# Kernel tuning notes

Measured on AMD Instinct MI355X. Metric: run time of the kernel, lower is better.

Reference implementation:

```python
import jax, jax.numpy as jnp
import numpy as np

MUL = 128          # multiplicity of 0e and 1o in left/output irreps
N_NODES = 131072   # graph nodes (batch dim)
INV_SQRT3 = 1.0 / np.sqrt(3.0)        # CG value for 0x1->1 and 1x1->0 (wigner 3j)
ALPHA = 1.0 / np.sqrt(2.0 * MUL)      # path_normalization='element': 2 paths of mul1*mul2=128 per output irrep
# effective per-instruction coefficients (CG * sqrt(2*l_out+1) component norm * ALPHA):
#   (0e,0e)->0e : 1 * 1 * ALPHA
#   (1o,1o)->0e : (1/sqrt(3)) * 1 * ALPHA
#   (0e,1o)->1o : (1/sqrt(3)) * sqrt(3) * ALPHA = ALPHA
#   (1o,0e)->1o : ALPHA


def setup_inputs() -> dict:
    key = jax.random.key(0)
    ks = jax.random.split(key, 7)
    x = jax.random.normal(ks[0], (N_NODES, 4 * MUL), jnp.float32)  # 128x0e + 128x1o -> dim 512
    y = jax.random.normal(ks[1], (N_NODES, 4), jnp.float32)        # 1x0e + 1x1o -> dim 4
    uni = lambda k: jax.random.uniform(k, (MUL, 1, MUL), jnp.float32, -1.0, 1.0)
    W1 = uni(ks[2])  # path (0e,0e)->0e
    W2 = uni(ks[3])  # path (0e,1o)->1o
    W3 = uni(ks[4])  # path (1o,0e)->1o
    W4 = uni(ks[5])  # path (1o,1o)->0e
    b = jax.random.uniform(ks[6], (MUL,), jnp.float32, -1.0, 1.0) / np.sqrt(MUL)
    return {"x": x, "y": y, "W1": W1, "W2": W2, "W3": W3, "W4": W4, "b": b}


def reference(x, y, W1, W2, W3, W4, b):
    n = x.shape[0]
    x0 = x[:, :MUL]                       # [N, 128]    scalars
    x1 = x[:, MUL:].reshape(n, MUL, 3)    # [N, 128, 3] vectors
    y0 = y[:, :1]                         # [N, 1]
    y1 = y[:, 1:].reshape(n, 1, 3)        # [N, 1, 3]
    # scalar output: (0e,0e)->0e and (1o,1o)->0e (inner product CG), plus bias
    out0 = ALPHA * (jnp.einsum('nu,nv,uvw->nw', x0, y0, W1)
                    + INV_SQRT3 * jnp.einsum('nui,nvi,uvw->nw', x1, y1, W4)) + b
    # vector output: (0e,1o)->1o and (1o,0e)->1o (identity CG)
    out1 = ALPHA * (jnp.einsum('nu,nvi,uvw->nwi', x0, y1, W2)
                    + jnp.einsum('nui,nv,uvw->nwi', x1, y0, W3))
    return jnp.concatenate([out0, out1.reshape(n, 3 * MUL)], axis=1)  # [N, 512]
```

## Files before the change

kernel.cpp:

```cpp
#include <hip/hip_runtime.h>

#define TILE_NODES 32
#define NBLOCKS 512

typedef __attribute__((ext_vector_type(4))) float f32x4;
typedef __attribute__((ext_vector_type(8))) __bf16 bf16x8;
typedef __attribute__((ext_vector_type(8))) unsigned short u16x8;

__device__ __forceinline__ unsigned short f2bf(float f) {
    unsigned u = __builtin_bit_cast(unsigned, f);
    u += 0x7fffu + ((u >> 16) & 1u);
    return (unsigned short)(u >> 16);
}

__global__ void build_bfrag_kernel(const float* __restrict__ W1,
                                   const float* __restrict__ W2,
                                   const float* __restrict__ W3,
                                   const float* __restrict__ W4,
                                   unsigned short* __restrict__ bfrag) {
    const float ALPHA = 0.0625f;
    const float A3    = 0.0625f * 0.57735026918962576f;
    int i = blockIdx.x * 256 + threadIdx.x;
    int j  = i & 7;
    int l  = (i >> 3) & 63;
    int ct = (i >> 9) & 7;
    int kt = (i >> 12) & 3;
    int T  = (i >> 14) & 3;
    int k   = kt * 32 + ((l >> 4) & 3) * 8 + j;
    int col = ct * 16 + (l & 15);
    const float* W = (T == 0) ? W1 : (T == 1) ? W2 : (T == 2) ? W3 : W4;
    float s = (T == 3) ? A3 : ALPHA;
    bfrag[i] = f2bf(s * W[k * 128 + col]);
}

__global__ __launch_bounds__(512, 2)
void o3tp_kernel(const float* __restrict__ x, const float* __restrict__ y,
                 const float* __restrict__ bias,
                 const unsigned short* __restrict__ bfrag,
                 float* __restrict__ out, int tiles_per_block) {
    __shared__ __align__(16) unsigned char smem[65536];
    const int tid = threadIdx.x;
    const int w   = tid >> 6;
    const int l   = tid & 63;
    const int lk  = l >> 4;
    const int lr  = l & 15;

    u16x8 bq[4][4];
    #pragma unroll
    for (int T = 0; T < 4; ++T)
        #pragma unroll
        for (int kt = 0; kt < 4; ++kt)
            bq[T][kt] = *(const u16x8*)(bfrag + (((T * 4 + kt) * 8 + w) << 9) + l * 8);
    const float bias_v = bias[w * 16 + lr];

    const int n_  = tid >> 4;
    const int G   = tid & 15;
    const int swz = (n_ & 7) << 4;

    const long tile0 = (long)blockIdx.x * tiles_per_block;

    f32x4 X0a, X0b, Ta, Tb, Tc, Td, Te, Tf;
    auto LOADS = [&](long tile) {
        const float* bp = x + (tile * TILE_NODES + n_) * 512;
        X0a = *(const f32x4*)(bp + 8 * G);
        X0b = *(const f32x4*)(bp + 8 * G + 4);
        const float* tp = bp + 128 + 24 * G;
        Ta = *(const f32x4*)(tp);      Tb = *(const f32x4*)(tp + 4);
        Tc = *(const f32x4*)(tp + 8);  Td = *(const f32x4*)(tp + 12);
        Te = *(const f32x4*)(tp + 16); Tf = *(const f32x4*)(tp + 20);
    };
    auto WRITE = [&](int buf) {
        unsigned char* base = smem + buf * 32768 + n_ * 256 + ((16 * G) ^ swz);
        u16x8 v;
        v[0] = f2bf(X0a[0]); v[1] = f2bf(X0a[1]); v[2] = f2bf(X0a[2]); v[3] = f2bf(X0a[3]);
        v[4] = f2bf(X0b[0]); v[5] = f2bf(X0b[1]); v[6] = f2bf(X0b[2]); v[7] = f2bf(X0b[3]);
        *(u16x8*)(base) = v;
        float t[24] = {Ta[0],Ta[1],Ta[2],Ta[3], Tb[0],Tb[1],Tb[2],Tb[3],
                       Tc[0],Tc[1],Tc[2],Tc[3], Td[0],Td[1],Td[2],Td[3],
                       Te[0],Te[1],Te[2],Te[3], Tf[0],Tf[1],Tf[2],Tf[3]};
        #pragma unroll
        for (int i3 = 0; i3 < 3; ++i3) {
            u16x8 u;
            #pragma unroll
            for (int up = 0; up < 8; ++up) u[up] = f2bf(t[3 * up + i3]);
            *(u16x8*)(base + (i3 + 1) * 8192) = u;
        }
    };

    LOADS(tile0);
    WRITE(0);

    for (int it = 0; it < tiles_per_block; ++it) {
        const long tile = tile0 + it;
        __syncthreads();
        if (it + 1 < tiles_per_block) LOADS(tile + 1);

        const unsigned char* ab = smem + (it & 1) * 32768;
        f32x4 M1[2] = {}, M2[2] = {}, M3[3][2] = {}, M4[3][2] = {};
        #pragma unroll
        for (int c = 0; c < 4; ++c) {
            u16x8 ar[2][4];
            #pragma unroll
            for (int m = 0; m < 2; ++m)
                #pragma unroll
                for (int kt = 0; kt < 4; ++kt)
                    ar[m][kt] = *(const u16x8*)(ab + c * 8192 + (m * 16 + lr) * 256
                                                + ((kt * 64 + lk * 16) ^ ((l & 7) << 4)));
            #pragma unroll
            for (int m = 0; m < 2; ++m)
                #pragma unroll
                for (int kt = 0; kt < 4; ++kt) {
                    if (c == 0) {
                        M1[m] = __builtin_amdgcn_mfma_f32_16x16x32_bf16(
                            __builtin_bit_cast(bf16x8, ar[m][kt]),
                            __builtin_bit_cast(bf16x8, bq[0][kt]), M1[m], 0, 0, 0);
                        M2[m] = __builtin_amdgcn_mfma_f32_16x16x32_bf16(
                            __builtin_bit_cast(bf16x8, ar[m][kt]),
                            __builtin_bit_cast(bf16x8, bq[1][kt]), M2[m], 0, 0, 0);
                    } else {
                        M3[c - 1][m] = __builtin_amdgcn_mfma_f32_16x16x32_bf16(
                            __builtin_bit_cast(bf16x8, ar[m][kt]),
                            __builtin_bit_cast(bf16x8, bq[2][kt]), M3[c - 1][m], 0, 0, 0);
                        M4[c - 1][m] = __builtin_amdgcn_mfma_f32_16x16x32_bf16(
                            __builtin_bit_cast(bf16x8, ar[m][kt]),
                            __builtin_bit_cast(bf16x8, bq[3][kt]), M4[c - 1][m], 0, 0, 0);
                    }
                }
        }

        const long nb = tile * TILE_NODES;
        #pragma unroll
        for (int m = 0; m < 2; ++m)
            #pragma unroll
            for (int j = 0; j < 4; ++j) {
                const int nl = m * 16 + lk * 4 + j;
                const f32x4 yv = *(const f32x4*)(y + (nb + nl) * 4);
                float* rp = out + (nb + nl) * 512;
                const int c0 = w * 16 + lr;
                rp[c0] = yv[0] * M1[m][j] + yv[1] * M4[0][m][j]
                       + yv[2] * M4[1][m][j] + yv[3] * M4[2][m][j] + bias_v;
                rp[128 + 3 * c0 + 0] = yv[1] * M2[m][j] + yv[0] * M3[0][m][j];
                rp[128 + 3 * c0 + 1] = yv[2] * M2[m][j] + yv[0] * M3[1][m][j];
                rp[128 + 3 * c0 + 2] = yv[3] * M2[m][j] + yv[0] * M3[2][m][j];
            }

        if (it + 1 < tiles_per_block) WRITE((it + 1) & 1);
    }
}

extern "C" void kernel_launch(void* const* d_in, const int* in_sizes, int n_in,
                              void* d_out, int out_size, void* d_ws, size_t ws_size,
                              hipStream_t stream) {
    const float* x  = (const float*)d_in[0];
    const float* y  = (const float*)d_in[1];
    const float* W1 = (const float*)d_in[2];
    const float* W2 = (const float*)d_in[3];
    const float* W3 = (const float*)d_in[4];
    const float* W4 = (const float*)d_in[5];
    const float* b  = (const float*)d_in[6];
    float* out = (float*)d_out;
    unsigned short* bfrag = (unsigned short*)d_ws;

    int n_nodes = in_sizes[0] / 512;
    int ntiles  = n_nodes / TILE_NODES;
    int tpb     = ntiles / NBLOCKS;

    hipLaunchKernelGGL(build_bfrag_kernel, dim3(256), dim3(256), 0, stream,
                       W1, W2, W3, W4, bfrag);
    hipLaunchKernelGGL(o3tp_kernel, dim3(NBLOCKS), dim3(512), 0, stream,
                       x, y, b, bfrag, out, tpb);
}
```

Baseline: 118.7 us.

## Defer output stores by one tile and use native bf16 conversion

Output values are now held in registers and stored at the start of the next iteration, so global stores overlap the next tile's MFMA work. The shared-memory write of the prefetched tile moves before the epilogue. Manual float-to-bf16 rounding is replaced with native __bf16 casts, which may map to hardware conversion instructions. Holding the outputs adds about 32 live registers, which could raise spilling risk under launch_bounds(512,2).

```diff
diff --git a/kernel.cpp b/kernel.cpp
--- a/kernel.cpp
+++ b/kernel.cpp
@@ -71,20 +71,39 @@
     };
     auto WRITE = [&](int buf) {
         unsigned char* base = smem + buf * 32768 + n_ * 256 + ((16 * G) ^ swz);
-        u16x8 v;
-        v[0] = f2bf(X0a[0]); v[1] = f2bf(X0a[1]); v[2] = f2bf(X0a[2]); v[3] = f2bf(X0a[3]);
-        v[4] = f2bf(X0b[0]); v[5] = f2bf(X0b[1]); v[6] = f2bf(X0b[2]); v[7] = f2bf(X0b[3]);
-        *(u16x8*)(base) = v;
+        bf16x8 v;
+        v[0] = (__bf16)X0a[0]; v[1] = (__bf16)X0a[1]; v[2] = (__bf16)X0a[2]; v[3] = (__bf16)X0a[3];
+        v[4] = (__bf16)X0b[0]; v[5] = (__bf16)X0b[1]; v[6] = (__bf16)X0b[2]; v[7] = (__bf16)X0b[3];
+        *(bf16x8*)(base) = v;
         float t[24] = {Ta[0],Ta[1],Ta[2],Ta[3], Tb[0],Tb[1],Tb[2],Tb[3],
                        Tc[0],Tc[1],Tc[2],Tc[3], Td[0],Td[1],Td[2],Td[3],
                        Te[0],Te[1],Te[2],Te[3], Tf[0],Tf[1],Tf[2],Tf[3]};
         #pragma unroll
         for (int i3 = 0; i3 < 3; ++i3) {
-            u16x8 u;
+            bf16x8 u;
             #pragma unroll
-            for (int up = 0; up < 8; ++up) u[up] = f2bf(t[3 * up + i3]);
-            *(u16x8*)(base + (i3 + 1) * 8192) = u;
+            for (int up = 0; up < 8; ++up) u[up] = (__bf16)t[3 * up + i3];
+            *(bf16x8*)(base + (i3 + 1) * 8192) = u;
         }
+    };
+
+    float ob0[2][4];
+    float ob1[2][4][3];
+    const int c0 = w * 16 + lr;
+
+    auto STORE_OUT = [&](long tile) {
+        const long nb = tile * TILE_NODES;
+        #pragma unroll
+        for (int m = 0; m < 2; ++m)
+            #pragma unroll
+            for (int j = 0; j < 4; ++j) {
+                const int nl = m * 16 + lk * 4 + j;
+                float* rp = out + (nb + nl) * 512;
+                rp[c0] = ob0[m][j];
+                rp[128 + 3 * c0 + 0] = ob1[m][j][0];
+                rp[128 + 3 * c0 + 1] = ob1[m][j][1];
+                rp[128 + 3 * c0 + 2] = ob1[m][j][2];
+            }
     };
 
     LOADS(tile0);
@@ -94,6 +113,7 @@
         const long tile = tile0 + it;
         __syncthreads();
         if (it + 1 < tiles_per_block) LOADS(tile + 1);
+        if (it > 0) STORE_OUT(tile - 1);
 
         const unsigned char* ab = smem + (it & 1) * 32768;
         f32x4 M1[2] = {}, M2[2] = {}, M3[3][2] = {}, M4[3][2] = {};
@@ -128,6 +148,8 @@
                 }
         }
 
+        if (it + 1 < tiles_per_block) WRITE((it + 1) & 1);
+
         const long nb = tile * TILE_NODES;
         #pragma unroll
         for (int m = 0; m < 2; ++m)
@@ -135,17 +157,14 @@
             for (int j = 0; j < 4; ++j) {
                 const int nl = m * 16 + lk * 4 + j;
                 const f32x4 yv = *(const f32x4*)(y + (nb + nl) * 4);
-                float* rp = out + (nb + nl) * 512;
-                const int c0 = w * 16 + lr;
-                rp[c0] = yv[0] * M1[m][j] + yv[1] * M4[0][m][j]
-                       + yv[2] * M4[1][m][j] + yv[3] * M4[2][m][j] + bias_v;
-                rp[128 + 3 * c0 + 0] = yv[1] * M2[m][j] + yv[0] * M3[0][m][j];
-                rp[128 + 3 * c0 + 1] = yv[2] * M2[m][j] + yv[0] * M3[1][m][j];
-                rp[128 + 3 * c0 + 2] = yv[3] * M2[m][j] + yv[0] * M3[2][m][j];
+                ob0[m][j] = yv[0] * M1[m][j] + yv[1] * M4[0][m][j]
+                          + yv[2] * M4[1][m][j] + yv[3] * M4[2][m][j] + bias_v;
+                ob1[m][j][0] = yv[1] * M2[m][j] + yv[0] * M3[0][m][j];
+                ob1[m][j][1] = yv[2] * M2[m][j] + yv[0] * M3[1][m][j];
+                ob1[m][j][2] = yv[3] * M2[m][j] + yv[0] * M3[2][m][j];
             }
-
-        if (it + 1 < tiles_per_block) WRITE((it + 1) & 1);
     }
+    STORE_OUT(tile0 + tiles_per_block - 1);
 }
 
 extern "C" void kernel_launch(void* const* d_in, const int* in_sizes, int n_in,
```

Result: slower. 123.1 us (+3.7%).

## Deepen prefetch pipeline, stage y in LDS, vectorize stores, halve block count

Applied to the files above, without the earlier changes.

Restructures the per-tile loop so global loads for tile it+2 are issued and the bf16 LDS write for tile it+1 happens before the epilogue stores, with a lighter lgkmcnt wait plus barrier replacing __syncthreads. The block's whole y slab is preloaded into extra LDS, the three vector outputs go out as one f32x3 store, and the hand-rolled bf16 rounding is swapped for native __bf16 conversion. The grid is halved to 256 blocks, each handling twice as many tiles. The larger LDS footprint and fewer blocks may reduce occupancy or leave CUs idle, and the custom wait/barrier relies on the compiler honouring sched_barrier ordering.

```diff
diff --git a/kernel.cpp b/kernel.cpp
--- a/kernel.cpp
+++ b/kernel.cpp
@@ -1,9 +1,10 @@
 #include <hip/hip_runtime.h>
 
 #define TILE_NODES 32
-#define NBLOCKS 512
+#define NBLOCKS 256
 
 typedef __attribute__((ext_vector_type(4))) float f32x4;
+typedef __attribute__((ext_vector_type(3))) float f32x3;
 typedef __attribute__((ext_vector_type(8))) __bf16 bf16x8;
 typedef __attribute__((ext_vector_type(8))) unsigned short u16x8;
 
@@ -38,7 +39,7 @@
                  const float* __restrict__ bias,
                  const unsigned short* __restrict__ bfrag,
                  float* __restrict__ out, int tiles_per_block) {
-    __shared__ __align__(16) unsigned char smem[65536];
+    __shared__ __align__(16) unsigned char smem[73728];
     const int tid = threadIdx.x;
     const int w   = tid >> 6;
     const int l   = tid & 63;
@@ -58,6 +59,11 @@
     const int swz = (n_ & 7) << 4;
 
     const long tile0 = (long)blockIdx.x * tiles_per_block;
+    const long node0 = tile0 * TILE_NODES;
+
+    float* yslab = (float*)(smem + 65536);
+    for (int i = tid; i < tiles_per_block * TILE_NODES; i += 512)
+        *(f32x4*)(yslab + i * 4) = *(const f32x4*)(y + (node0 + i) * 4);
 
     f32x4 X0a, X0b, Ta, Tb, Tc, Td, Te, Tf;
     auto LOADS = [&](long tile) {
@@ -71,29 +77,32 @@
     };
     auto WRITE = [&](int buf) {
         unsigned char* base = smem + buf * 32768 + n_ * 256 + ((16 * G) ^ swz);
-        u16x8 v;
-        v[0] = f2bf(X0a[0]); v[1] = f2bf(X0a[1]); v[2] = f2bf(X0a[2]); v[3] = f2bf(X0a[3]);
-        v[4] = f2bf(X0b[0]); v[5] = f2bf(X0b[1]); v[6] = f2bf(X0b[2]); v[7] = f2bf(X0b[3]);
-        *(u16x8*)(base) = v;
+        bf16x8 v;
+        v[0] = (__bf16)X0a[0]; v[1] = (__bf16)X0a[1]; v[2] = (__bf16)X0a[2]; v[3] = (__bf16)X0a[3];
+        v[4] = (__bf16)X0b[0]; v[5] = (__bf16)X0b[1]; v[6] = (__bf16)X0b[2]; v[7] = (__bf16)X0b[3];
+        *(bf16x8*)(base) = v;
         float t[24] = {Ta[0],Ta[1],Ta[2],Ta[3], Tb[0],Tb[1],Tb[2],Tb[3],
                        Tc[0],Tc[1],Tc[2],Tc[3], Td[0],Td[1],Td[2],Td[3],
                        Te[0],Te[1],Te[2],Te[3], Tf[0],Tf[1],Tf[2],Tf[3]};
         #pragma unroll
         for (int i3 = 0; i3 < 3; ++i3) {
-            u16x8 u;
+            bf16x8 u;
             #pragma unroll
-            for (int up = 0; up < 8; ++up) u[up] = f2bf(t[3 * up + i3]);
-            *(u16x8*)(base + (i3 + 1) * 8192) = u;
+            for (int up = 0; up < 8; ++up) u[up] = (__bf16)t[3 * up + i3];
+            *(bf16x8*)(base + (i3 + 1) * 8192) = u;
         }
     };
 
+    const int c0 = w * 16 + lr;
+
     LOADS(tile0);
     WRITE(0);
+    if (tiles_per_block > 1) LOADS(tile0 + 1);
+    asm volatile("s_waitcnt lgkmcnt(0)" ::: "memory");
+    __builtin_amdgcn_s_barrier();
 
     for (int it = 0; it < tiles_per_block; ++it) {
         const long tile = tile0 + it;
-        __syncthreads();
-        if (it + 1 < tiles_per_block) LOADS(tile + 1);
 
         const unsigned char* ab = smem + (it & 1) * 32768;
         f32x4 M1[2] = {}, M2[2] = {}, M3[3][2] = {}, M4[3][2] = {};
@@ -128,23 +137,30 @@
                 }
         }
 
-        const long nb = tile * TILE_NODES;
+        if (it + 1 < tiles_per_block) WRITE((it + 1) & 1);
+        if (it + 2 < tiles_per_block) LOADS(tile + 2);
+        __builtin_amdgcn_sched_barrier(0);
+
         #pragma unroll
         for (int m = 0; m < 2; ++m)
             #pragma unroll
             for (int j = 0; j < 4; ++j) {
                 const int nl = m * 16 + lk * 4 + j;
-                const f32x4 yv = *(const f32x4*)(y + (nb + nl) * 4);
-                float* rp = out + (nb + nl) * 512;
-                const int c0 = w * 16 + lr;
+                const f32x4 yv = *(const f32x4*)(yslab + (it * TILE_NODES + nl) * 4);
+                float* rp = out + (node0 + it * TILE_NODES + nl) * 512;
                 rp[c0] = yv[0] * M1[m][j] + yv[1] * M4[0][m][j]
                        + yv[2] * M4[1][m][j] + yv[3] * M4[2][m][j] + bias_v;
-                rp[128 + 3 * c0 + 0] = yv[1] * M2[m][j] + yv[0] * M3[0][m][j];
-                rp[128 + 3 * c0 + 1] = yv[2] * M2[m][j] + yv[0] * M3[1][m][j];
-                rp[128 + 3 * c0 + 2] = yv[3] * M2[m][j] + yv[0] * M3[2][m][j];
+                f32x3 o1;
+                o1[0] = yv[1] * M2[m][j] + yv[0] * M3[0][m][j];
+                o1[1] = yv[2] * M2[m][j] + yv[0] * M3[1][m][j];
+                o1[2] = yv[3] * M2[m][j] + yv[0] * M3[2][m][j];
+                *(f32x3*)(rp + 128 + 3 * c0) = o1;
             }
 
-        if (it + 1 < tiles_per_block) WRITE((it + 1) & 1);
+        if (it + 1 < tiles_per_block) {
+            asm volatile("s_waitcnt lgkmcnt(0)" ::: "memory");
+            __builtin_amdgcn_s_barrier();
+        }
     }
 }
 
```

Result: no change. 119.1 us (median of 2 runs) (+0.3%).
